# Kernel tuning notes

Hardware: AMD Instinct MI355X
Metric: run time of the kernel (lower is better)

Reference implementation:

```python
import jax, jax.numpy as jnp
import numpy as np

N_SRC = 20000
N_TAR = 20000
DIM = 3


def setup_inputs() -> dict:
    key = jax.random.key(0)
    k1, k2 = jax.random.split(key)
    src_V = jax.random.normal(k1, (N_SRC, DIM), dtype=jnp.float32)
    tar_V = jax.random.normal(k2, (N_TAR, DIM), dtype=jnp.float32)
    return {"src_V": src_V, "tar_V": tar_V}


def reference(src_V, tar_V):
    # Brute-force 1-NN replacing the CPU cKDTree query.
    # Squared distances: ||t||^2 - 2 t.s^T + ||s||^2  -> [M, N]
    d2 = (
        jnp.sum(tar_V * tar_V, axis=1, keepdims=True)
        - 2.0 * (tar_V @ src_V.T)
        + jnp.sum(src_V * src_V, axis=1)[None, :]
    )
    ii = jnp.argmin(d2, axis=1)          # nearest src index per tar point
    diff = src_V[ii] - tar_V             # gather + residual, [M, 3]
    return 0.5 * jnp.sum(diff * diff)
```

## Files before the change

### kernel.cpp

```cpp
#include <hip/hip_runtime.h>
#include <float.h>

#define N_SRC 20000
#define N_TAR 20000
#define TPB 256
#define SPLITS 12
#define TILES 54
#define SRC_PAD (SPLITS * TILES * 32)
#define TGRP 79
#define TAR_PAD (TGRP * TPB)
#define FBLOCKS ((N_TAR + 255) / 256)

typedef _Float16 half8 __attribute__((ext_vector_type(8)));
typedef float floatx16 __attribute__((ext_vector_type(16)));


#define DPP_MIN(v, ctrl) { \
    const int _s = __builtin_amdgcn_update_dpp( \
        __float_as_int(v), __float_as_int(v), (ctrl), 0xf, 0xf, false); \
    v = fminf(v, __int_as_float(_s)); }
#define COL_REDUCE(v) { \
    DPP_MIN(v, 0xB1)   \
    DPP_MIN(v, 0x4E)   \
    DPP_MIN(v, 0x141)  \
    DPP_MIN(v, 0x140)  \
    DPP_MIN(v, 0x142)  }

__global__ __launch_bounds__(TPB) void nn_prep(
    const float* __restrict__ src, const float* __restrict__ tar,
    half8* __restrict__ pack, half8* __restrict__ apack,
    float* __restrict__ out)
{
    const int i = blockIdx.x * TPB + threadIdx.x;
    if (i == 0) out[0] = 0.f;

    if (i < SRC_PAD) {
        half8 f0 = {0, 0, 0, 0, 0, 0, 0, 0};
        half8 f1 = {0, (_Float16)30000.f, 0, 0, 0, 0, 0, 0};
        if (i < N_SRC) {
            const float x = src[i * 3 + 0];
            const float y = src[i * 3 + 1];
            const float z = src[i * 3 + 2];
            const _Float16 xh = (_Float16)x, yh = (_Float16)y, zh = (_Float16)z;
            const _Float16 xl = (_Float16)(x - (float)xh);
            const _Float16 yl = (_Float16)(y - (float)yh);
            const _Float16 zl = (_Float16)(z - (float)zh);
            const float nrm = 0.5f * (x * x + y * y + z * z);
            const _Float16 nh = (_Float16)nrm;
            const _Float16 nl = (_Float16)(nrm - (float)nh);
            f0 = (half8){xh, yh, zh, xh, yh, zh, xl, yl};
            f1 = (half8){zl, nh, nl, 0, 0, 0, 0, 0};
        }
        pack[i * 2 + 0] = f0;
        pack[i * 2 + 1] = f1;
    }

    if (i < TAR_PAD) {
        const int t = min(i, N_TAR - 1);
        const float tx = tar[t * 3 + 0];
        const float ty = tar[t * 3 + 1];
        const float tz = tar[t * 3 + 2];
        const _Float16 txh = (_Float16)tx, tyh = (_Float16)ty, tzh = (_Float16)tz;
        const _Float16 txl = (_Float16)(tx - (float)txh);
        const _Float16 tyl = (_Float16)(ty - (float)tyh);
        const _Float16 tzl = (_Float16)(tz - (float)tzh);
        apack[i * 2 + 0] = (half8){-txh, -tyh, -tzh, -txl, -tyl, -tzl, -txh, -tyh};
        apack[i * 2 + 1] = (half8){-tzh, (_Float16)1.f, (_Float16)1.f, 0, 0, 0, 0, 0};
    }
}

__global__ __launch_bounds__(TPB, 4) void nn_mfma(
    const half8* __restrict__ pack, const half8* __restrict__ apack,
    float* __restrict__ part)
{
    const int tid  = threadIdx.x;
    const int lane = tid & 63;
    const int col  = lane & 31;
    const int half = (lane >> 5) & 1;
    const int wave = tid >> 6;

    const int strip0 = (blockIdx.x * 4 + wave) * 2;
    const half8 a0 = apack[strip0 * 64 + col * 2 + half];
    const half8 a1 = apack[(strip0 + 1) * 64 + col * 2 + half];

    const int sbase = blockIdx.y * (TILES * 32);
    const half8* bp = pack + (size_t)(sbase + col) * 2 + half;

    floatx16 m0, m1;
#pragma unroll
    for (int i = 0; i < 16; ++i) { m0[i] = FLT_MAX; m1[i] = FLT_MAX; }
    const floatx16 zero = {};

    half8 r0 = bp[0 * 64];
    half8 r1 = bp[1 * 64];
    half8 r2 = bp[2 * 64];
    half8 r3 = bp[3 * 64];
#pragma unroll 1
    for (int tp = 0; tp < TILES; tp += 2) {
        const int nx = min(tp + 4, TILES - 2);
        const half8 n0 = bp[nx * 64];
        const half8 n1 = bp[nx * 64 + 64];
        {
            const floatx16 d00 = __builtin_amdgcn_mfma_f32_32x32x16_f16(a0, r0, zero, 0, 0, 0);
            const floatx16 d01 = __builtin_amdgcn_mfma_f32_32x32x16_f16(a0, r1, zero, 0, 0, 0);
#pragma unroll
            for (int i = 0; i < 16; ++i) m0[i] = fminf(m0[i], fminf(d00[i], d01[i]));
        }
        {
            const floatx16 d10 = __builtin_amdgcn_mfma_f32_32x32x16_f16(a1, r0, zero, 0, 0, 0);
            const floatx16 d11 = __builtin_amdgcn_mfma_f32_32x32x16_f16(a1, r1, zero, 0, 0, 0);
#pragma unroll
            for (int i = 0; i < 16; ++i) m1[i] = fminf(m1[i], fminf(d10[i], d11[i]));
        }
        r0 = r2; r1 = r3; r2 = n0; r3 = n1;
    }

#pragma unroll
    for (int i = 0; i < 16; ++i) { COL_REDUCE(m0[i]) COL_REDUCE(m1[i]) }

    if (col == 16) {
        float* prow = part + (size_t)blockIdx.y * N_TAR;
#pragma unroll
        for (int i = 0; i < 16; ++i) {
            const int row = (i & 3) + 8 * (i >> 2) + 4 * half;
            const int t0 = min(strip0 * 32 + row, N_TAR - 1);
            const int t1 = min((strip0 + 1) * 32 + row, N_TAR - 1);
            prow[t0] = m0[i];
            prow[t1] = m1[i];
        }
    }
}

__global__ __launch_bounds__(256) void nn_finalize(
    const float* __restrict__ tar, const float* __restrict__ part,
    float* __restrict__ out)
{
    const int t = blockIdx.x * 256 + threadIdx.x;
    float contrib = 0.f;
    if (t < N_TAR) {
        float m = FLT_MAX;
#pragma unroll
        for (int c = 0; c < SPLITS; ++c) m = fminf(m, part[c * N_TAR + t]);
        const float tx = tar[t * 3 + 0];
        const float ty = tar[t * 3 + 1];
        const float tz = tar[t * 3 + 2];
        contrib = 0.5f * (tx * tx + ty * ty + tz * tz) + m;
    }
    for (int off = 32; off > 0; off >>= 1)
        contrib += __shfl_down(contrib, off);
    __shared__ float red[4];
    if ((threadIdx.x & 63) == 0) red[threadIdx.x >> 6] = contrib;
    __syncthreads();
    if (threadIdx.x == 0) {
        float s = 0.f;
#pragma unroll
        for (int w = 0; w < 4; ++w) s += red[w];
        atomicAdd(out, s);
    }
}

extern "C" void kernel_launch(void* const* d_in, const int* in_sizes, int n_in,
                              void* d_out, int out_size, void* d_ws, size_t ws_size,
                              hipStream_t stream) {
    const float* src = (const float*)d_in[0];
    const float* tar = (const float*)d_in[1];
    float* out = (float*)d_out;

    char* w = (char*)d_ws;
    float* part  = (float*)w;
    half8* pack  = (half8*)(w + 1024 * 1024);
    half8* apack = (half8*)(w + 2 * 1024 * 1024);

    nn_prep<<<(SRC_PAD + TPB - 1) / TPB, TPB, 0, stream>>>(src, tar, pack, apack, out);
    dim3 grid1(TGRP, SPLITS);
    nn_mfma<<<grid1, TPB, 0, stream>>>(pack, apack, part);
    nn_finalize<<<FBLOCKS, 256, 0, stream>>>(tar, part, out);
}
```

Before: 79.49 us.

## Stage source tiles in LDS and build target fragments inside MFMA kernel

```diff
diff --git a/kernel.cpp b/kernel.cpp
--- a/kernel.cpp
+++ b/kernel.cpp
@@ -4,11 +4,10 @@
 #define N_SRC 20000
 #define N_TAR 20000
 #define TPB 256
-#define SPLITS 12
-#define TILES 54
-#define SRC_PAD (SPLITS * TILES * 32)
+#define SPLITS 16
+#define TILES 42
+#define PACK_N (SPLITS * TILES * 64)
 #define TGRP 79
-#define TAR_PAD (TGRP * TPB)
 #define FBLOCKS ((N_TAR + 255) / 256)
 
 typedef _Float16 half8 __attribute__((ext_vector_type(8)));
@@ -27,36 +26,61 @@
     DPP_MIN(v, 0x142)  }
 
 __global__ __launch_bounds__(TPB) void nn_prep(
-    const float* __restrict__ src, const float* __restrict__ tar,
-    half8* __restrict__ pack, half8* __restrict__ apack,
+    const float* __restrict__ src, half8* __restrict__ pack,
     float* __restrict__ out)
 {
     const int i = blockIdx.x * TPB + threadIdx.x;
     if (i == 0) out[0] = 0.f;
+    if (i >= PACK_N) return;
 
-    if (i < SRC_PAD) {
-        half8 f0 = {0, 0, 0, 0, 0, 0, 0, 0};
-        half8 f1 = {0, (_Float16)30000.f, 0, 0, 0, 0, 0, 0};
-        if (i < N_SRC) {
-            const float x = src[i * 3 + 0];
-            const float y = src[i * 3 + 1];
-            const float z = src[i * 3 + 2];
-            const _Float16 xh = (_Float16)x, yh = (_Float16)y, zh = (_Float16)z;
+    const int L = i & 63;
+    const int hf = L >> 5;
+    const int s = (i >> 6) * 32 + (L & 31);
+
+    half8 f = {0, 0, 0, 0, 0, 0, 0, 0};
+    if (s < N_SRC) {
+        const float x = src[s * 3 + 0];
+        const float y = src[s * 3 + 1];
+        const float z = src[s * 3 + 2];
+        const _Float16 xh = (_Float16)x, yh = (_Float16)y, zh = (_Float16)z;
+        if (hf == 0) {
             const _Float16 xl = (_Float16)(x - (float)xh);
             const _Float16 yl = (_Float16)(y - (float)yh);
+            f = (half8){xh, yh, zh, xh, yh, zh, xl, yl};
+        } else {
             const _Float16 zl = (_Float16)(z - (float)zh);
             const float nrm = 0.5f * (x * x + y * y + z * z);
             const _Float16 nh = (_Float16)nrm;
             const _Float16 nl = (_Float16)(nrm - (float)nh);
-            f0 = (half8){xh, yh, zh, xh, yh, zh, xl, yl};
-            f1 = (half8){zl, nh, nl, 0, 0, 0, 0, 0};
+            f = (half8){zl, nh, nl, 0, 0, 0, 0, 0};
         }
-        pack[i * 2 + 0] = f0;
-        pack[i * 2 + 1] = f1;
+    } else if (hf == 1) {
+        f = (half8){0, (_Float16)30000.f, 0, 0, 0, 0, 0, 0};
     }
+    pack[i] = f;
+}
 
-    if (i < TAR_PAD) {
-        const int t = min(i, N_TAR - 1);
+__global__ __launch_bounds__(TPB, 4) void nn_mfma(
+    const half8* __restrict__ pack, const float* __restrict__ tar,
+    float* __restrict__ part)
+{
+    __shared__ half8 lds[TILES * 64];
+
+    const int tid  = threadIdx.x;
+    const int lane = tid & 63;
+    const int col  = lane & 31;
+    const int half = (lane >> 5) & 1;
+    const int wave = tid >> 6;
+
+    const half8* gp = pack + (size_t)blockIdx.y * (TILES * 64);
+    for (int g = tid; g < TILES * 64; g += TPB) lds[g] = pack[(size_t)blockIdx.y * (TILES * 64) + g];
+    (void)gp;
+
+    const int strip0 = (blockIdx.x * 4 + wave) * 2;
+    half8 a0, a1;
+#pragma unroll
+    for (int sidx = 0; sidx < 2; ++sidx) {
+        const int t = min((strip0 + sidx) * 32 + col, N_TAR - 1);
         const float tx = tar[t * 3 + 0];
         const float ty = tar[t * 3 + 1];
         const float tz = tar[t * 3 + 2];
@@ -64,42 +88,31 @@
         const _Float16 txl = (_Float16)(tx - (float)txh);
         const _Float16 tyl = (_Float16)(ty - (float)tyh);
         const _Float16 tzl = (_Float16)(tz - (float)tzh);
-        apack[i * 2 + 0] = (half8){-txh, -tyh, -tzh, -txl, -tyl, -tzl, -txh, -tyh};
-        apack[i * 2 + 1] = (half8){-tzh, (_Float16)1.f, (_Float16)1.f, 0, 0, 0, 0, 0};
+        half8 a;
+        if (half == 0)
+            a = (half8){-txh, -tyh, -tzh, -txl, -tyl, -tzl, -txh, -tyh};
+        else
+            a = (half8){-tzh, (_Float16)1.f, (_Float16)1.f, 0, 0, 0, 0, 0};
+        if (sidx == 0) a0 = a; else a1 = a;
     }
-}
 
-__global__ __launch_bounds__(TPB, 4) void nn_mfma(
-    const half8* __restrict__ pack, const half8* __restrict__ apack,
-    float* __restrict__ part)
-{
-    const int tid  = threadIdx.x;
-    const int lane = tid & 63;
-    const int col  = lane & 31;
-    const int half = (lane >> 5) & 1;
-    const int wave = tid >> 6;
-
-    const int strip0 = (blockIdx.x * 4 + wave) * 2;
-    const half8 a0 = apack[strip0 * 64 + col * 2 + half];
-    const half8 a1 = apack[(strip0 + 1) * 64 + col * 2 + half];
-
-    const int sbase = blockIdx.y * (TILES * 32);
-    const half8* bp = pack + (size_t)(sbase + col) * 2 + half;
+    __syncthreads();
 
     floatx16 m0, m1;
 #pragma unroll
     for (int i = 0; i < 16; ++i) { m0[i] = FLT_MAX; m1[i] = FLT_MAX; }
     const floatx16 zero = {};
 
-    half8 r0 = bp[0 * 64];
-    half8 r1 = bp[1 * 64];
-    half8 r2 = bp[2 * 64];
-    half8 r3 = bp[3 * 64];
+    const half8* lp = lds + lane;
+    half8 r0 = lp[0 * 64];
+    half8 r1 = lp[1 * 64];
+    half8 r2 = lp[2 * 64];
+    half8 r3 = lp[3 * 64];
 #pragma unroll 1
     for (int tp = 0; tp < TILES; tp += 2) {
         const int nx = min(tp + 4, TILES - 2);
-        const half8 n0 = bp[nx * 64];
-        const half8 n1 = bp[nx * 64 + 64];
+        const half8 n0 = lp[nx * 64];
+        const half8 n1 = lp[nx * 64 + 64];
         {
             const floatx16 d00 = __builtin_amdgcn_mfma_f32_32x32x16_f16(a0, r0, zero, 0, 0, 0);
             const floatx16 d01 = __builtin_amdgcn_mfma_f32_32x32x16_f16(a0, r1, zero, 0, 0, 0);
@@ -167,12 +180,11 @@
     float* out = (float*)d_out;
 
     char* w = (char*)d_ws;
-    float* part  = (float*)w;
-    half8* pack  = (half8*)(w + 1024 * 1024);
-    half8* apack = (half8*)(w + 2 * 1024 * 1024);
+    float* part = (float*)w;
+    half8* pack = (half8*)(w + 2 * 1024 * 1024);
 
-    nn_prep<<<(SRC_PAD + TPB - 1) / TPB, TPB, 0, stream>>>(src, tar, pack, apack, out);
+    nn_prep<<<(PACK_N + TPB - 1) / TPB, TPB, 0, stream>>>(src, pack, out);
     dim3 grid1(TGRP, SPLITS);
-    nn_mfma<<<grid1, TPB, 0, stream>>>(pack, apack, part);
+    nn_mfma<<<grid1, TPB, 0, stream>>>(pack, tar, part);
     nn_finalize<<<FBLOCKS, 256, 0, stream>>>(tar, part, out);
 }
```

Result: slower. 89.36 us (+12.4%).
